# Kernel optimization log

Hardware: AMD Instinct MI355X
Metric: run time of the kernel (lower is better)

Reference implementation:

```python
import jax, jax.numpy as jnp
import numpy as np

D = 512            # d_model
H = 4              # num_heads
DK = D // 2        # total key dim (expand_k = 0.5)
DV = D             # total value dim (expand_v = 1.0)
HK = DK // H       # per-head key dim  = 64
HV = DV // H       # per-head value dim = 128
GATE_LOW_RANK = 16
GATE_LOGIT_NORMALIZER = 16.0
LN_EPS = 1e-5


def setup_inputs() -> dict:
    key = jax.random.key(0)
    ks = jax.random.split(key, 9)
    B, S = 2, 16384
    g = lambda k, shape, scale: (jax.random.normal(k, shape, dtype=jnp.float32) * scale)
    return {
        "x":    g(ks[0], (B, S, D), 1.0),
        "Wq":   g(ks[1], (D, DK), D ** -0.5),
        "Wk":   g(ks[2], (D, DK), D ** -0.5),
        "Wv":   g(ks[3], (D, DV), D ** -0.5),
        "Wg":   g(ks[4], (D, DV), D ** -0.5),
        "Wgk1": g(ks[5], (D, GATE_LOW_RANK), D ** -0.5),
        "Wgk2": g(ks[6], (GATE_LOW_RANK, DK), GATE_LOW_RANK ** -0.5),
        "bgk2": jnp.zeros((DK,), jnp.float32),
        "Wo":   g(ks[7], (DV, D), DV ** -0.5),
    }


def _gla(x, Wq, Wk, Wv, Wg, Wgk1, Wgk2, bgk2, Wo):
    B, S, _ = x.shape
    q = (x @ Wq).reshape(B, S, H, HK) * (HK ** -0.5)   # [B,S,H,HK]
    k = (x @ Wk).reshape(B, S, H, HK)
    v = (x @ Wv).reshape(B, S, H, HV)
    g = (x @ Wg).reshape(B, S, H, HV)                  # output gate
    # low-rank forget gate, in log space
    gk = jax.nn.log_sigmoid((x @ Wgk1) @ Wgk2 + bgk2) / GATE_LOGIT_NORMALIZER
    gk = gk.reshape(B, S, H, HK)

    # gated linear recurrence over time:
    #   h_t = diag(exp(gk_t)) h_{t-1} + k_t^T v_t ;  o_t = q_t h_t
    def step(h, inp):
        q_t, k_t, v_t, gk_t = inp                      # [B,H,HK] / [B,H,HV]
        h = jnp.exp(gk_t)[..., None] * h + k_t[..., None] * v_t[..., None, :]
        o_t = jnp.einsum('bhk,bhkv->bhv', q_t, h)
        return h, o_t

    h0 = jnp.zeros((B, H, HK, HV), x.dtype)
    xs = (q.swapaxes(0, 1), k.swapaxes(0, 1), v.swapaxes(0, 1), gk.swapaxes(0, 1))
    _, o = jax.lax.scan(step, h0, xs)                  # o: [S,B,H,HV]
    o = o.swapaxes(0, 1)                               # [B,S,H,HV]

    # per-head LayerNorm (no affine) + swish output gate
    mu = o.mean(-1, keepdims=True)
    var = ((o - mu) ** 2).mean(-1, keepdims=True)
    o = (o - mu) * jax.lax.rsqrt(var + LN_EPS)
    o = o * jax.nn.silu(g)
    return o.reshape(B, S, DV) @ Wo                    # [B,S,D]


def reference(x, Wq, Wk, Wv, Wg, Wgk1, Wgk2, bgk2, Wo):
    return _gla(x, Wq, Wk, Wv, Wg, Wgk1, Wgk2, bgk2, Wo)
```

## Files before the change

kernel.cpp:

```cpp
#include <hip/hip_runtime.h>
#include <hip/hip_bf16.h>


typedef __hip_bfloat16 bf16;
typedef _Float16 f16;
typedef _Float16 half8 __attribute__((ext_vector_type(8)));
typedef float f32x4 __attribute__((ext_vector_type(4)));
typedef short short8 __attribute__((ext_vector_type(8)));

#define DEV static __device__ __forceinline__

DEV float b2f(bf16 v) { return __bfloat162float(v); }
DEV bf16 f2b(float v) { return __float2bfloat16(v); }
DEV float bits2f(unsigned int u16) {
    union { unsigned int u; float f; } c; c.u = u16 << 16; return c.f;
}
DEV short f2bs(float v) {
    union { bf16 h; short s; } u; u.h = __float2bfloat16(v); return u.s;
}
DEV unsigned short f2bu(float v) {
    union { bf16 h; unsigned short s; } u; u.h = __float2bfloat16(v); return u.s;
}
DEV float fast_rcp(float v) { return __builtin_amdgcn_rcpf(v); }

DEV float ldf(const float* p) { return *p; }
DEV float ldf(const bf16* p) { return b2f(*p); }
DEV void stf(float* p, float v) { *p = v; }
DEV void stf(bf16* p, float v) { *p = f2b(v); }

DEV float4 ld4(const float* p) { return *(const float4*)p; }
DEV float4 ld4(const bf16* p) {
    const uint2 r = *(const uint2*)p;
    return make_float4(bits2f(r.x & 0xffffu), bits2f(r.x >> 16),
                       bits2f(r.y & 0xffffu), bits2f(r.y >> 16));
}

DEV half8 ld8h(const float* p) {
    const float4 a = *(const float4*)p, b = *(const float4*)(p + 4);
    half8 h;
    h[0] = (f16)a.x; h[1] = (f16)a.y; h[2] = (f16)a.z; h[3] = (f16)a.w;
    h[4] = (f16)b.x; h[5] = (f16)b.y; h[6] = (f16)b.z; h[7] = (f16)b.w;
    return h;
}
DEV half8 ld8h(const f16* p) { return *(const half8*)p; }
DEV half8 ld8h(const bf16* p) {
    const float4 a = ld4(p), b = ld4(p + 4);
    half8 h;
    h[0] = (f16)a.x; h[1] = (f16)a.y; h[2] = (f16)a.z; h[3] = (f16)a.w;
    h[4] = (f16)b.x; h[5] = (f16)b.y; h[6] = (f16)b.z; h[7] = (f16)b.w;
    return h;
}

DEV f32x4 mfma_bf(short8 a, short8 b, f32x4 c) {
    return __builtin_amdgcn_mfma_f32_16x16x32_bf16(a, b, c, 0, 0, 0);
}
DEV f32x4 mfma_h(half8 a, half8 b, f32x4 c) {
    return __builtin_amdgcn_mfma_f32_16x16x32_f16(a, b, c, 0, 0, 0);
}

DEV size_t voff(int v, int t) {
    return (size_t)(((((v >> 4) * 2 + (t >> 5)) * 4 + ((t >> 3) & 3)) * 16
                     + (v & 15)) * 8 + (t & 7));
}

__global__ __launch_bounds__(256) void cvt_xh_k(
    const float* __restrict__ x, f16* __restrict__ xh)
{
    const size_t i = ((size_t)blockIdx.x * 256 + threadIdx.x) * 8;
    *(half8*)&xh[i] = ld8h(&x[i]);
}

__global__ __launch_bounds__(256) void cvt_wt_k(
    const float* __restrict__ Wq, const float* __restrict__ Wk,
    const float* __restrict__ Wv, const float* __restrict__ Wg,
    const float* __restrict__ Wo, f16* __restrict__ Wt)
{
    __shared__ float tile[64][65];
    const int nb = blockIdx.x * 64;
    const int tid = threadIdx.x;
    const float* src; int nloc, N;
    if (nb < 256)       { src = Wq; N = 256; nloc = nb; }
    else if (nb < 512)  { src = Wk; N = 256; nloc = nb - 256; }
    else if (nb < 1024) { src = Wv; N = 512; nloc = nb - 512; }
    else if (nb < 1536) { src = Wg; N = 512; nloc = nb - 1024; }
    else                { src = Wo; N = 512; nloc = nb - 1536; }
    for (int k0 = 0; k0 < 512; k0 += 64) {
        for (int e = tid; e < 4096; e += 256) {
            const int i = e >> 6, j = e & 63;
            tile[i][j] = src[(size_t)(k0 + i) * N + nloc + j];
        }
        __syncthreads();
        for (int e = tid; e < 4096; e += 256) {
            const int j = e >> 6, i = e & 63;
            Wt[(size_t)(nb + j) * 512 + k0 + i] = (f16)tile[i][j];
        }
        __syncthreads();
    }
}

__global__ __launch_bounds__(256) void proj_gemm_k(
    const f16* __restrict__ A, const f16* __restrict__ Wt,
    bf16* __restrict__ Qb, bf16* __restrict__ Kb,
    bf16* __restrict__ VF, bf16* __restrict__ GOb)
{
    __shared__ __align__(16) f16 As[128][40];
    __shared__ __align__(16) f16 Bs[128][40];
    const int bm = blockIdx.x * 128;
    const int bn = blockIdx.y * 128;
    const int tid = threadIdx.x;
    const int lane = tid & 63;
    const int wid = tid >> 6;
    const int wr = wid >> 1, wc = wid & 1;
    const int al = lane & 15;
    const int kg = lane >> 4;

    f32x4 acc[4][4];
#pragma unroll
    for (int m = 0; m < 4; ++m)
#pragma unroll
        for (int n = 0; n < 4; ++n)
#pragma unroll
            for (int r = 0; r < 4; ++r) acc[m][n][r] = 0.f;

    const int ar = tid >> 1;
    const int ac = (tid & 1) * 16;

    for (int k0 = 0; k0 < 512; k0 += 32) {
        {
            const f16* ap = A + (size_t)(bm + ar) * 512 + k0 + ac;
            *(half8*)&As[ar][ac] = *(const half8*)ap;
            *(half8*)&As[ar][ac + 8] = *(const half8*)(ap + 8);
        }
        {
            const f16* bp = Wt + (size_t)(bn + ar) * 512 + k0 + ac;
            *(half8*)&Bs[ar][ac] = *(const half8*)bp;
            *(half8*)&Bs[ar][ac + 8] = *(const half8*)(bp + 8);
        }
        __syncthreads();
        half8 af[4], bfr[4];
#pragma unroll
        for (int m = 0; m < 4; ++m)
            af[m] = *(const half8*)&As[wr * 64 + m * 16 + al][kg * 8];
#pragma unroll
        for (int n = 0; n < 4; ++n)
            bfr[n] = *(const half8*)&Bs[wc * 64 + n * 16 + al][kg * 8];
#pragma unroll
        for (int m = 0; m < 4; ++m)
#pragma unroll
            for (int n = 0; n < 4; ++n)
                acc[m][n] = mfma_h(af[m], bfr[n], acc[m][n]);
        __syncthreads();
    }

    const int r00 = bm + wr * 64 + kg * 4;
    const int c00 = bn + wc * 64 + al;
    const int seg = bn >> 8;
    if (seg == 0) {
#pragma unroll
        for (int m = 0; m < 4; ++m)
#pragma unroll
            for (int n = 0; n < 4; ++n)
#pragma unroll
                for (int r = 0; r < 4; ++r)
                    stf(&Qb[(size_t)(r00 + m * 16 + r) * 256 + c00 + n * 16],
                        acc[m][n][r] * 0.125f);
    } else if (seg == 1) {
#pragma unroll
        for (int m = 0; m < 4; ++m)
#pragma unroll
            for (int n = 0; n < 4; ++n)
#pragma unroll
                for (int r = 0; r < 4; ++r)
                    stf(&Kb[(size_t)(r00 + m * 16 + r) * 256 + (c00 - 256) + n * 16],
                        acc[m][n][r]);
    } else if (seg <= 3) {
#pragma unroll
        for (int m = 0; m < 4; ++m) {
            const int row0 = r00 + m * 16;
            const int bi = row0 >> 14;
            const int chunk = (row0 >> 6) & 255;
            const int tc = row0 & 63;
#pragma unroll
            for (int n = 0; n < 4; ++n) {
                const int col = c00 - 512 + n * 16;
                const int h = col >> 7, v = col & 127;
                bf16* dst = VF + (size_t)((bi * 4 + h) * 256 + chunk) * 8192
                               + voff(v, tc);
                ushort4 pk;
                pk.x = f2bu(acc[m][n][0]); pk.y = f2bu(acc[m][n][1]);
                pk.z = f2bu(acc[m][n][2]); pk.w = f2bu(acc[m][n][3]);
                *(ushort4*)dst = pk;
            }
        }
    } else {
#pragma unroll
        for (int m = 0; m < 4; ++m)
#pragma unroll
            for (int n = 0; n < 4; ++n)
#pragma unroll
                for (int r = 0; r < 4; ++r) {
                    const float v = acc[m][n][r];
                    const float sil = v * fast_rcp(1.f + __expf(-v));
                    stf(&GOb[(size_t)(r00 + m * 16 + r) * 512 + (c00 - 1024) + n * 16],
                        sil);
                }
    }
}

__global__ __launch_bounds__(256) void gemm_bt_k(
    const bf16* __restrict__ A, const f16* __restrict__ Bt,
    float* __restrict__ C, int M, int N, int K)
{
    __shared__ __align__(16) f16 As[128][40];
    __shared__ __align__(16) f16 Bs[128][40];
    const int bm = blockIdx.x * 128;
    const int bn = blockIdx.y * 128;
    const int tid = threadIdx.x;
    const int lane = tid & 63;
    const int wid = tid >> 6;
    const int wr = wid >> 1, wc = wid & 1;
    const int al = lane & 15;
    const int kg = lane >> 4;

    f32x4 acc[4][4];
#pragma unroll
    for (int m = 0; m < 4; ++m)
#pragma unroll
        for (int n = 0; n < 4; ++n)
#pragma unroll
            for (int r = 0; r < 4; ++r) acc[m][n][r] = 0.f;

    const int ar = tid >> 1;
    const int ac = (tid & 1) * 16;

    for (int k0 = 0; k0 < K; k0 += 32) {
        {
            const bf16* ap = A + (size_t)(bm + ar) * K + k0 + ac;
            *(half8*)&As[ar][ac] = ld8h(ap);
            *(half8*)&As[ar][ac + 8] = ld8h(ap + 8);
        }
        {
            const f16* bp = Bt + (size_t)(bn + ar) * K + k0 + ac;
            *(half8*)&Bs[ar][ac] = *(const half8*)bp;
            *(half8*)&Bs[ar][ac + 8] = *(const half8*)(bp + 8);
        }
        __syncthreads();
        half8 af[4], bfr[4];
#pragma unroll
        for (int m = 0; m < 4; ++m)
            af[m] = *(const half8*)&As[wr * 64 + m * 16 + al][kg * 8];
#pragma unroll
        for (int n = 0; n < 4; ++n)
            bfr[n] = *(const half8*)&Bs[wc * 64 + n * 16 + al][kg * 8];
#pragma unroll
        for (int m = 0; m < 4; ++m)
#pragma unroll
            for (int n = 0; n < 4; ++n)
                acc[m][n] = mfma_h(af[m], bfr[n], acc[m][n]);
        __syncthreads();
    }
    const int r0 = bm + wr * 64 + kg * 4;
    const int c0 = bn + wc * 64 + al;
#pragma unroll
    for (int m = 0; m < 4; ++m)
#pragma unroll
        for (int n = 0; n < 4; ++n)
#pragma unroll
            for (int r = 0; r < 4; ++r)
                C[(size_t)(r0 + m * 16 + r) * N + c0 + n * 16] = acc[m][n][r];
}

template <typename GKT>
__global__ __launch_bounds__(256) void gate_mfma_k(
    const f16* __restrict__ xh, const float* __restrict__ Wgk1,
    const float* __restrict__ Wgk2, const float* __restrict__ bgk2,
    GKT* __restrict__ GK)
{
    __shared__ __align__(16) f16 As[128][40];
    __shared__ __align__(16) f16 w1s[16][520];
    __shared__ float tls[128][17];
    const int bm = blockIdx.x * 128;
    const int tid = threadIdx.x;
    const int lane = tid & 63;
    const int wid = tid >> 6;
    const int al = lane & 15;
    const int kg = lane >> 4;
    const int kg8 = kg * 8;

    for (int e = tid; e < 8192; e += 256) {
        const int kk = e >> 4, n = e & 15;
        w1s[n][kk] = (f16)Wgk1[e];
    }

    f32x4 acc[2];
#pragma unroll
    for (int m = 0; m < 2; ++m)
#pragma unroll
        for (int r = 0; r < 4; ++r) acc[m][r] = 0.f;

    const int ar = tid >> 1;
    const int ac = (tid & 1) * 16;
    for (int k0 = 0; k0 < 512; k0 += 32) {
        {
            const f16* ap = xh + (size_t)(bm + ar) * 512 + k0 + ac;
            *(half8*)&As[ar][ac] = *(const half8*)ap;
            *(half8*)&As[ar][ac + 8] = *(const half8*)(ap + 8);
        }
        __syncthreads();
        const half8 bfr = *(const half8*)&w1s[al][k0 + kg8];
#pragma unroll
        for (int m = 0; m < 2; ++m) {
            const half8 af = *(const half8*)&As[wid * 32 + m * 16 + al][kg8];
            acc[m] = mfma_h(af, bfr, acc[m]);
        }
        __syncthreads();
    }
#pragma unroll
    for (int m = 0; m < 2; ++m)
#pragma unroll
        for (int r = 0; r < 4; ++r)
            tls[wid * 32 + m * 16 + kg * 4 + r][al] = acc[m][r];
    __syncthreads();

    float w2[16];
#pragma unroll
    for (int r = 0; r < 16; ++r) w2[r] = Wgk2[r * 256 + tid];
    const float bb = bgk2[tid];
    GKT* gout = GK + (size_t)bm * 256 + tid;
    for (int m = 0; m < 128; ++m) {
        float z = bb;
#pragma unroll
        for (int r = 0; r < 16; ++r) z = fmaf(tls[m][r], w2[r], z);
        const float ls = fminf(z, 0.f) - __logf(1.f + __expf(-fabsf(z)));
        stf(&gout[(size_t)m * 256], ls * (1.f / 16.f));
    }
}

template <typename GKT, typename CST>
__global__ __launch_bounds__(256) void chunk_state_k(
    const bf16* __restrict__ Km, const bf16* __restrict__ VF,
    const GKT* __restrict__ GKm, CST* __restrict__ CS,
    float* __restrict__ DD)
{
    __shared__ __align__(16) short k2t[64][72];
    __shared__ float cpart[4][64];
    const int blk = blockIdx.x;
    const int chunk = blk & 255;
    const int bh = blk >> 8;
    const int bi = bh >> 2, h = bh & 3;
    const int rowbase = bi * 16384 + chunk * 64;
    const int tid = threadIdx.x;
    const int k = tid & 63, tg = tid >> 6;

    float g[16];
    {
        float run = 0.f;
#pragma unroll
        for (int j = 0; j < 16; ++j) {
            run += ldf(&GKm[(size_t)(rowbase + tg * 16 + j) * 256 + h * 64 + k]);
            g[j] = run;
        }
        cpart[tg][k] = run;
    }
    __syncthreads();
    float off = 0.f;
#pragma unroll
    for (int s = 0; s < 3; ++s) if (s < tg) off += cpart[s][k];
    const float tot = cpart[0][k] + cpart[1][k] + cpart[2][k] + cpart[3][k];
    if (tg == 0) DD[(size_t)blk * 64 + k] = __expf(tot);

    {
        short8 p0, p1;
#pragma unroll
        for (int j = 0; j < 16; ++j) {
            const float kv = ldf(&Km[(size_t)(rowbase + tg * 16 + j) * 256 + h * 64 + k]);
            const float w = kv * __expf(tot - (g[j] + off));
            if (j < 8) p0[j] = f2bs(w); else p1[j - 8] = f2bs(w);
        }
        *(short8*)&k2t[k][tg * 16] = p0;
        *(short8*)&k2t[k][tg * 16 + 8] = p1;
    }
    __syncthreads();

    const int lane = tid & 63, wid = tid >> 6;
    const int al = lane & 15, kg = lane >> 4, kg8 = kg * 8;
    const bf16* Vtb = VF + (size_t)blk * 8192;

    short8 xf[2][2];
#pragma unroll
    for (int m = 0; m < 2; ++m)
#pragma unroll
        for (int ks = 0; ks < 2; ++ks)
            xf[m][ks] = *(const short8*)&Vtb[(size_t)(((wid * 2 + m) * 2 + ks) * 64 + lane) * 8];
    short8 yf[2][4];
#pragma unroll
    for (int ks = 0; ks < 2; ++ks)
#pragma unroll
        for (int n = 0; n < 4; ++n)
            yf[ks][n] = *(const short8*)&k2t[n * 16 + al][ks * 32 + kg8];

    f32x4 acc[2][4];
#pragma unroll
    for (int m = 0; m < 2; ++m)
#pragma unroll
        for (int n = 0; n < 4; ++n)
#pragma unroll
            for (int r = 0; r < 4; ++r) acc[m][n][r] = 0.f;
#pragma unroll
    for (int ks = 0; ks < 2; ++ks)
#pragma unroll
        for (int m = 0; m < 2; ++m)
#pragma unroll
            for (int n = 0; n < 4; ++n)
                acc[m][n] = mfma_bf(xf[m][ks], yf[ks][n], acc[m][n]);

    CST* out = CS + (size_t)blk * 8192;
#pragma unroll
    for (int m = 0; m < 2; ++m)
#pragma unroll
        for (int n = 0; n < 4; ++n)
#pragma unroll
            for (int r = 0; r < 4; ++r)
                stf(&out[(size_t)(wid * 32 + m * 16 + kg * 4 + r) * 64 + n * 16 + al],
                    acc[m][n][r]);
}

template <typename CST>
__global__ __launch_bounds__(256) void scan_k(
    const CST* __restrict__ CS, const float* __restrict__ DD,
    bf16* __restrict__ HF)
{
    const int bh = blockIdx.x >> 5;
    const int slice = blockIdx.x & 31;
    const int tid = threadIdx.x;
    const int e = slice * 256 + tid;
    const int v = e >> 6, k = e & 63;
    float H = 0.f;
    const CST* base = CS + (size_t)bh * 256 * 8192 + e;
    bf16* hbase = HF + (size_t)bh * 256 * 8192 + voff(v, k);
    const float* dbase = DD + (size_t)bh * 256 * 64 + k;
#pragma unroll 4
    for (int n = 0; n < 256; ++n) {
        const float s = ldf(&base[(size_t)n * 8192]);
        const float d = dbase[(size_t)n * 64];
        stf(&hbase[(size_t)n * 8192], H);
        H = fmaf(d, H, s);
    }
}

template <typename GKT>
__global__ __launch_bounds__(256) void chunk_out_k(
    const bf16* __restrict__ Qm, const bf16* __restrict__ Km,
    const bf16* __restrict__ VF, const GKT* __restrict__ GKm,
    const bf16* __restrict__ HF, bf16* GO)
{
    __shared__ __align__(16) short qs[64][72];
    __shared__ __align__(16) short ks[64][72];
    __shared__ __align__(16) short ab[64][72];
    __shared__ float cpart[4][64];

    const int blk = blockIdx.x;
    const int chunk = blk & 255;
    const int bh = blk >> 8;
    const int bi = bh >> 2, h = bh & 3;
    const int rowbase = bi * 16384 + chunk * 64;
    const int tid = threadIdx.x;
    const int k = tid & 63, tg = tid >> 6;

    float g[16];
    {
        float run = 0.f;
#pragma unroll
        for (int j = 0; j < 16; ++j) {
            run += ldf(&GKm[(size_t)(rowbase + tg * 16 + j) * 256 + h * 64 + k]);
            g[j] = run;
        }
        cpart[tg][k] = run;
    }
    __syncthreads();
    float off = 0.f;
#pragma unroll
    for (int s = 0; s < 3; ++s) if (s < tg) off += cpart[s][k];

#pragma unroll
    for (int j = 0; j < 16; ++j) {
        const int t = tg * 16 + j;
        const size_t idx = (size_t)(rowbase + t) * 256 + h * 64 + k;
        const float gc = g[j] + off;
        const float eg = __expf(gc);
        qs[t][k] = f2bs(ldf(&Qm[idx]) * eg);
        ks[t][k] = f2bs(ldf(&Km[idx]) * fast_rcp(eg));
    }
    __syncthreads();

    const int lane = tid & 63, wid = tid >> 6;
    const int al = lane & 15, kg = lane >> 4;
    const int w16 = wid * 16, kg8 = kg * 8;

    short8 xq[2];
    xq[0] = *(const short8*)&qs[w16 + al][kg8];
    xq[1] = *(const short8*)&qs[w16 + al][32 + kg8];

    f32x4 aacc[4];
#pragma unroll
    for (int n = 0; n < 4; ++n)
#pragma unroll
        for (int r = 0; r < 4; ++r) aacc[n][r] = 0.f;
#pragma unroll
    for (int ksb = 0; ksb < 2; ++ksb)
#pragma unroll
        for (int n = 0; n < 4; ++n) {
            const short8 y = *(const short8*)&ks[n * 16 + al][ksb * 32 + kg8];
            aacc[n] = mfma_bf(xq[ksb], y, aacc[n]);
        }
#pragma unroll
    for (int n = 0; n < 4; ++n)
#pragma unroll
        for (int r = 0; r < 4; ++r) {
            const int tt = w16 + kg * 4 + r;
            const int ii = n * 16 + al;
            ab[tt][ii] = (ii <= tt) ? f2bs(aacc[n][r]) : (short)0;
        }
    short8 xa[2];
    xa[0] = *(const short8*)&ab[w16 + al][kg8];
    xa[1] = *(const short8*)&ab[w16 + al][32 + kg8];

    const bf16* Vtb = VF + (size_t)blk * 8192;
    const bf16* Hb = HF + (size_t)blk * 8192;
    f32x4 oacc[8];
#pragma unroll
    for (int n = 0; n < 8; ++n)
#pragma unroll
        for (int r = 0; r < 4; ++r) oacc[n][r] = 0.f;
#pragma unroll
    for (int n = 0; n < 8; ++n) {
        const size_t f0 = (size_t)((n * 2 + 0) * 64 + lane) * 8;
        const size_t f1 = (size_t)((n * 2 + 1) * 64 + lane) * 8;
        const short8 yv0 = *(const short8*)&Vtb[f0];
        const short8 yv1 = *(const short8*)&Vtb[f1];
        const short8 yh0 = *(const short8*)&Hb[f0];
        const short8 yh1 = *(const short8*)&Hb[f1];
        oacc[n] = mfma_bf(xa[0], yv0, oacc[n]);
        oacc[n] = mfma_bf(xa[1], yv1, oacc[n]);
        oacc[n] = mfma_bf(xq[0], yh0, oacc[n]);
        oacc[n] = mfma_bf(xq[1], yh1, oacc[n]);
    }

    float psum[4] = {0.f, 0.f, 0.f, 0.f}, psq[4] = {0.f, 0.f, 0.f, 0.f};
#pragma unroll
    for (int n = 0; n < 8; ++n)
#pragma unroll
        for (int r = 0; r < 4; ++r) {
            const float v = oacc[n][r];
            psum[r] += v; psq[r] = fmaf(v, v, psq[r]);
        }
#pragma unroll
    for (int offx = 1; offx < 16; offx <<= 1)
#pragma unroll
        for (int r = 0; r < 4; ++r) {
            psum[r] += __shfl_xor(psum[r], offx);
            psq[r] += __shfl_xor(psq[r], offx);
        }
#pragma unroll
    for (int r = 0; r < 4; ++r) {
        const float mu = psum[r] * (1.f / 128.f);
        const float var = psq[r] * (1.f / 128.f) - mu * mu;
        const float rstd = rsqrtf(fmaxf(var, 0.f) + 1e-5f);
        const int row = rowbase + w16 + kg * 4 + r;
        bf16* gop = GO + (size_t)row * 512 + h * 128 + al;
#pragma unroll
        for (int n = 0; n < 8; ++n) {
            const float sil = b2f(gop[n * 16]);
            gop[n * 16] = f2b((oacc[n][r] - mu) * rstd * sil);
        }
    }
}

__global__ __launch_bounds__(256) void zero_k(float* out, int n) {
    const int i = blockIdx.x * 256 + threadIdx.x;
    if (i < n) out[i] = 0.f;
}

template <typename GKT, typename CST>
static void run_all(const float* x, const float* Wq, const float* Wk,
                    const float* Wv, const float* Wg, const float* Wgk1,
                    const float* Wgk2, const float* bgk2, const float* Wo,
                    float* out, char* ws, hipStream_t stream)
{
    const int M = 32768;
    auto aln = [](size_t v) { return (v + 255) & ~(size_t)255; };
    char* cur = ws;
    bf16* Qb = (bf16*)cur;  cur += aln((size_t)M * 256 * 2);
    bf16* Kb = (bf16*)cur;  cur += aln((size_t)M * 256 * 2);
    bf16* Vfb = (bf16*)cur; cur += aln((size_t)M * 512 * 2);
    bf16* GOb = (bf16*)cur; cur += aln((size_t)M * 512 * 2);
    bf16* Hfb = (bf16*)cur; cur += aln((size_t)2048 * 8192 * 2);
    float* DDb = (float*)cur; cur += aln((size_t)2048 * 64 * 4);
    f16* Wtb = (f16*)cur;   cur += aln((size_t)2048 * 512 * 2);
    GKT* GKb = (GKT*)cur;   cur += aln((size_t)M * 256 * sizeof(GKT));
    CST* CSb = (CST*)cur;
    f16* xh = (f16*)CSb;

    const dim3 blk(256);
    cvt_xh_k<<<dim3(8192), blk, 0, stream>>>(x, xh);
    cvt_wt_k<<<dim3(32), blk, 0, stream>>>(Wq, Wk, Wv, Wg, Wo, Wtb);
    proj_gemm_k<<<dim3(M / 128, 12), blk, 0, stream>>>(xh, Wtb, Qb, Kb, Vfb, GOb);
    gate_mfma_k<<<dim3(M / 128), blk, 0, stream>>>(xh, Wgk1, Wgk2, bgk2, GKb);
    chunk_state_k<<<dim3(2048), blk, 0, stream>>>(Kb, Vfb, GKb, CSb, DDb);
    scan_k<<<dim3(256), blk, 0, stream>>>(CSb, DDb, Hfb);
    chunk_out_k<<<dim3(2048), blk, 0, stream>>>(Qb, Kb, Vfb, GKb, Hfb, GOb);
    gemm_bt_k<<<dim3(M / 128, 4), blk, 0, stream>>>(GOb, Wtb + (size_t)1536 * 512,
                                                    out, M, 512, 512);
}

extern "C" void kernel_launch(void* const* d_in, const int* in_sizes, int n_in,
                              void* d_out, int out_size, void* d_ws, size_t ws_size,
                              hipStream_t stream)
{
    const float* x    = (const float*)d_in[0];
    const float* Wq   = (const float*)d_in[1];
    const float* Wk   = (const float*)d_in[2];
    const float* Wv   = (const float*)d_in[3];
    const float* Wg   = (const float*)d_in[4];
    const float* Wgk1 = (const float*)d_in[5];
    const float* Wgk2 = (const float*)d_in[6];
    const float* bgk2 = (const float*)d_in[7];
    const float* Wo   = (const float*)d_in[8];
    float* out = (float*)d_out;

    const size_t M = 32768;
    const size_t slack = 8192;
    const size_t base = 2 * M * 256 * 2 + 2 * M * 512 * 2
                      + (size_t)2048 * 8192 * 2 + 2048 * 64 * 4
                      + (size_t)2048 * 512 * 2 + slack;
    const size_t gk_f = M * 256 * 4, gk_b = M * 256 * 2;
    const size_t cs_f = (size_t)2048 * 8192 * 4, cs_b = (size_t)2048 * 8192 * 2;
    const size_t needA = base + gk_f + cs_f;
    const size_t needB = base + gk_b + cs_b;

    if (ws_size >= needA) {
        run_all<float, float>(x, Wq, Wk, Wv, Wg, Wgk1, Wgk2, bgk2, Wo,
                              out, (char*)d_ws, stream);
    } else if (ws_size >= needB) {
        run_all<bf16, bf16>(x, Wq, Wk, Wv, Wg, Wgk1, Wgk2, bgk2, Wo,
                            out, (char*)d_ws, stream);
    } else {
        zero_k<<<dim3((out_size + 255) / 256), dim3(256), 0, stream>>>(out, out_size);
    }
}
```

Measured before the change: 389.4 us.

## Use direct global-to-LDS loads with XOR swizzle in projection GEMMs

Both the input projection GEMM and the output projection GEMM now stage tiles with global_load_lds 16-byte direct-to-LDS loads. They use a K=64 step and an XOR-swizzled unpadded LDS layout, which cuts register round-trips and the number of barriers. The gated output is now written as fp16 instead of bf16, so the output GEMM can load its A operand directly without converting bf16 to f16. Sizes are hardcoded to 512, and the output buffer is reinterpreted as f16, which narrows the value range to f16 limits.

```diff
diff --git a/kernel.cpp b/kernel.cpp
--- a/kernel.cpp
+++ b/kernel.cpp
@@ -20,6 +20,9 @@
 }
 DEV unsigned short f2bu(float v) {
     union { bf16 h; unsigned short s; } u; u.h = __float2bfloat16(v); return u.s;
+}
+DEV short f2hs(float v) {
+    union { f16 h; short s; } u; u.h = (f16)v; return u.s;
 }
 DEV float fast_rcp(float v) { return __builtin_amdgcn_rcpf(v); }
 
@@ -43,19 +46,18 @@
     return h;
 }
 DEV half8 ld8h(const f16* p) { return *(const half8*)p; }
-DEV half8 ld8h(const bf16* p) {
-    const float4 a = ld4(p), b = ld4(p + 4);
-    half8 h;
-    h[0] = (f16)a.x; h[1] = (f16)a.y; h[2] = (f16)a.z; h[3] = (f16)a.w;
-    h[4] = (f16)b.x; h[5] = (f16)b.y; h[6] = (f16)b.z; h[7] = (f16)b.w;
-    return h;
-}
 
 DEV f32x4 mfma_bf(short8 a, short8 b, f32x4 c) {
     return __builtin_amdgcn_mfma_f32_16x16x32_bf16(a, b, c, 0, 0, 0);
 }
 DEV f32x4 mfma_h(half8 a, half8 b, f32x4 c) {
     return __builtin_amdgcn_mfma_f32_16x16x32_f16(a, b, c, 0, 0, 0);
+}
+
+DEV void gl_lds16(const f16* g, f16* l) {
+    __builtin_amdgcn_global_load_lds(
+        (const __attribute__((address_space(1))) void*)g,
+        (__attribute__((address_space(3))) void*)l, 16, 0, 0);
 }
 
 DEV size_t voff(int v, int t) {
@@ -103,8 +105,8 @@
     bf16* __restrict__ Qb, bf16* __restrict__ Kb,
     bf16* __restrict__ VF, bf16* __restrict__ GOb)
 {
-    __shared__ __align__(16) f16 As[128][40];
-    __shared__ __align__(16) f16 Bs[128][40];
+    __shared__ __align__(16) f16 As[128][64];
+    __shared__ __align__(16) f16 Bs[128][64];
     const int bm = blockIdx.x * 128;
     const int bn = blockIdx.y * 128;
     const int tid = threadIdx.x;
@@ -113,6 +115,7 @@
     const int wr = wid >> 1, wc = wid & 1;
     const int al = lane & 15;
     const int kg = lane >> 4;
+    const int al7 = al & 7;
 
     f32x4 acc[4][4];
 #pragma unroll
@@ -122,34 +125,35 @@
 #pragma unroll
             for (int r = 0; r < 4; ++r) acc[m][n][r] = 0.f;
 
-    const int ar = tid >> 1;
-    const int ac = (tid & 1) * 16;
-
-    for (int k0 = 0; k0 < 512; k0 += 32) {
-        {
-            const f16* ap = A + (size_t)(bm + ar) * 512 + k0 + ac;
-            *(half8*)&As[ar][ac] = *(const half8*)ap;
-            *(half8*)&As[ar][ac + 8] = *(const half8*)(ap + 8);
-        }
-        {
-            const f16* bp = Wt + (size_t)(bn + ar) * 512 + k0 + ac;
-            *(half8*)&Bs[ar][ac] = *(const half8*)bp;
-            *(half8*)&Bs[ar][ac + 8] = *(const half8*)(bp + 8);
+    const int srow = wid * 32 + (lane >> 3);
+    const int sswz = ((lane & 7) ^ (lane >> 3)) << 3;
+    const f16* ap = A + (size_t)(bm + srow) * 512 + sswz;
+    const f16* bp = Wt + (size_t)(bn + srow) * 512 + sswz;
+
+    for (int k0 = 0; k0 < 512; k0 += 64) {
+        if (k0) __syncthreads();
+#pragma unroll
+        for (int i = 0; i < 4; ++i) {
+            gl_lds16(ap + (size_t)i * 8 * 512 + k0, &As[wid * 32 + i * 8][0]);
+            gl_lds16(bp + (size_t)i * 8 * 512 + k0, &Bs[wid * 32 + i * 8][0]);
         }
         __syncthreads();
-        half8 af[4], bfr[4];
-#pragma unroll
-        for (int m = 0; m < 4; ++m)
-            af[m] = *(const half8*)&As[wr * 64 + m * 16 + al][kg * 8];
-#pragma unroll
-        for (int n = 0; n < 4; ++n)
-            bfr[n] = *(const half8*)&Bs[wc * 64 + n * 16 + al][kg * 8];
-#pragma unroll
-        for (int m = 0; m < 4; ++m)
+#pragma unroll
+        for (int ks = 0; ks < 2; ++ks) {
+            half8 af[4], bfr[4];
+            const int sp = ((ks * 4 + kg) ^ al7) << 3;
+#pragma unroll
+            for (int m = 0; m < 4; ++m)
+                af[m] = *(const half8*)&As[wr * 64 + m * 16 + al][sp];
 #pragma unroll
             for (int n = 0; n < 4; ++n)
-                acc[m][n] = mfma_h(af[m], bfr[n], acc[m][n]);
-        __syncthreads();
+                bfr[n] = *(const half8*)&Bs[wc * 64 + n * 16 + al][sp];
+#pragma unroll
+            for (int m = 0; m < 4; ++m)
+#pragma unroll
+                for (int n = 0; n < 4; ++n)
+                    acc[m][n] = mfma_h(af[m], bfr[n], acc[m][n]);
+        }
     }
 
     const int r00 = bm + wr * 64 + kg * 4;
@@ -208,11 +212,11 @@
 }
 
 __global__ __launch_bounds__(256) void gemm_bt_k(
-    const bf16* __restrict__ A, const f16* __restrict__ Bt,
-    float* __restrict__ C, int M, int N, int K)
-{
-    __shared__ __align__(16) f16 As[128][40];
-    __shared__ __align__(16) f16 Bs[128][40];
+    const f16* __restrict__ A, const f16* __restrict__ Bt,
+    float* __restrict__ C)
+{
+    __shared__ __align__(16) f16 As[128][64];
+    __shared__ __align__(16) f16 Bs[128][64];
     const int bm = blockIdx.x * 128;
     const int bn = blockIdx.y * 128;
     const int tid = threadIdx.x;
@@ -221,6 +225,7 @@
     const int wr = wid >> 1, wc = wid & 1;
     const int al = lane & 15;
     const int kg = lane >> 4;
+    const int al7 = al & 7;
 
     f32x4 acc[4][4];
 #pragma unroll
@@ -230,34 +235,35 @@
 #pragma unroll
             for (int r = 0; r < 4; ++r) acc[m][n][r] = 0.f;
 
-    const int ar = tid >> 1;
-    const int ac = (tid & 1) * 16;
-
-    for (int k0 = 0; k0 < K; k0 += 32) {
-        {
-            const bf16* ap = A + (size_t)(bm + ar) * K + k0 + ac;
-            *(half8*)&As[ar][ac] = ld8h(ap);
-            *(half8*)&As[ar][ac + 8] = ld8h(ap + 8);
-        }
-        {
-            const f16* bp = Bt + (size_t)(bn + ar) * K + k0 + ac;
-            *(half8*)&Bs[ar][ac] = *(const half8*)bp;
-            *(half8*)&Bs[ar][ac + 8] = *(const half8*)(bp + 8);
+    const int srow = wid * 32 + (lane >> 3);
+    const int sswz = ((lane & 7) ^ (lane >> 3)) << 3;
+    const f16* ap = A + (size_t)(bm + srow) * 512 + sswz;
+    const f16* bp = Bt + (size_t)(bn + srow) * 512 + sswz;
+
+    for (int k0 = 0; k0 < 512; k0 += 64) {
+        if (k0) __syncthreads();
+#pragma unroll
+        for (int i = 0; i < 4; ++i) {
+            gl_lds16(ap + (size_t)i * 8 * 512 + k0, &As[wid * 32 + i * 8][0]);
+            gl_lds16(bp + (size_t)i * 8 * 512 + k0, &Bs[wid * 32 + i * 8][0]);
         }
         __syncthreads();
-        half8 af[4], bfr[4];
-#pragma unroll
-        for (int m = 0; m < 4; ++m)
-            af[m] = *(const half8*)&As[wr * 64 + m * 16 + al][kg * 8];
-#pragma unroll
-        for (int n = 0; n < 4; ++n)
-            bfr[n] = *(const half8*)&Bs[wc * 64 + n * 16 + al][kg * 8];
-#pragma unroll
-        for (int m = 0; m < 4; ++m)
+#pragma unroll
+        for (int ks = 0; ks < 2; ++ks) {
+            half8 af[4], bfr[4];
+            const int sp = ((ks * 4 + kg) ^ al7) << 3;
+#pragma unroll
+            for (int m = 0; m < 4; ++m)
+                af[m] = *(const half8*)&As[wr * 64 + m * 16 + al][sp];
 #pragma unroll
             for (int n = 0; n < 4; ++n)
-                acc[m][n] = mfma_h(af[m], bfr[n], acc[m][n]);
-        __syncthreads();
+                bfr[n] = *(const half8*)&Bs[wc * 64 + n * 16 + al][sp];
+#pragma unroll
+            for (int m = 0; m < 4; ++m)
+#pragma unroll
+                for (int n = 0; n < 4; ++n)
+                    acc[m][n] = mfma_h(af[m], bfr[n], acc[m][n]);
+        }
     }
     const int r0 = bm + wr * 64 + kg * 4;
     const int c0 = bn + wc * 64 + al;
@@ -267,7 +273,7 @@
         for (int n = 0; n < 4; ++n)
 #pragma unroll
             for (int r = 0; r < 4; ++r)
-                C[(size_t)(r0 + m * 16 + r) * N + c0 + n * 16] = acc[m][n][r];
+                C[(size_t)(r0 + m * 16 + r) * 512 + c0 + n * 16] = acc[m][n][r];
 }
 
 template <typename GKT>
@@ -567,11 +573,12 @@
         const float var = psq[r] * (1.f / 128.f) - mu * mu;
         const float rstd = rsqrtf(fmaxf(var, 0.f) + 1e-5f);
         const int row = rowbase + w16 + kg * 4 + r;
-        bf16* gop = GO + (size_t)row * 512 + h * 128 + al;
+        short* gop = (short*)(GO + (size_t)row * 512 + h * 128 + al);
 #pragma unroll
         for (int n = 0; n < 8; ++n) {
-            const float sil = b2f(gop[n * 16]);
-            gop[n * 16] = f2b((oacc[n][r] - mu) * rstd * sil);
+            const bf16 gb = *(const bf16*)&gop[n * 16];
+            const float sil = b2f(gb);
+            gop[n * 16] = f2hs((oacc[n][r] - mu) * rstd * sil);
         }
     }
 }
@@ -609,8 +616,8 @@
     chunk_state_k<<<dim3(2048), blk, 0, stream>>>(Kb, Vfb, GKb, CSb, DDb);
     scan_k<<<dim3(256), blk, 0, stream>>>(CSb, DDb, Hfb);
     chunk_out_k<<<dim3(2048), blk, 0, stream>>>(Qb, Kb, Vfb, GKb, Hfb, GOb);
-    gemm_bt_k<<<dim3(M / 128, 4), blk, 0, stream>>>(GOb, Wtb + (size_t)1536 * 512,
-                                                    out, M, 512, 512);
+    gemm_bt_k<<<dim3(M / 128, 4), blk, 0, stream>>>((const f16*)GOb,
+                                                    Wtb + (size_t)1536 * 512, out);
 }
 
 extern "C" void kernel_launch(void* const* d_in, const int* in_sizes, int n_in,
```

After: 368.9 us. 5.3% less time.
